# Optimization experiments

Measured on AMD Instinct MI355X. Metric: run time of the kernel, lower is better.

## Reference

```python
import jax, jax.numpy as jnp
import numpy as np

BETA = 0.25


def setup_inputs() -> dict:
    key = jax.random.key(0)
    k1, k2 = jax.random.split(key)
    z = jax.random.normal(k1, (16, 1024, 256), dtype=jnp.float32)
    embedding = jax.random.normal(k2, (8192, 256), dtype=jnp.float32)
    return {"z": z, "embedding": embedding}


def reference(z, embedding):
    e_dim = embedding.shape[-1]
    z_flat = jnp.reshape(z, (-1, e_dim))  # [N, e_dim]
    # d[i,k] = ||z_i||^2 + ||e_k||^2 - 2 z_i . e_k  -> [N, n_e]
    d = (jnp.sum(z_flat ** 2, axis=1, keepdims=True)
         + jnp.sum(embedding ** 2, axis=1)
         - 2.0 * jnp.einsum('nd,kd->nk', z_flat, embedding))
    min_encoding_indices = jnp.argmin(d, axis=1)  # [N]
    z_q = embedding[min_encoding_indices]
    z_q = jnp.reshape(z_q, z.shape)
    loss = (jnp.mean((jax.lax.stop_gradient(z_q) - z) ** 2)
            + BETA * jnp.mean((z_q - jax.lax.stop_gradient(z)) ** 2))
    z_q = z + jax.lax.stop_gradient(z_q - z)  # straight-through estimator
    return (z_q, loss, min_encoding_indices)
```

## Files before the change

kernel.cpp:

```cpp
#include <hip/hip_runtime.h>
#include <stdint.h>

#define N_ROWS   16384
#define DIM      256
#define N_CODES  8192
#define ZQ_ELEMS 4194304

typedef _Float16 f16x8 __attribute__((ext_vector_type(8)));
typedef _Float16 f16x4 __attribute__((ext_vector_type(4)));
typedef float    f32x16 __attribute__((ext_vector_type(16)));
typedef unsigned long long u64;

#define WS_ET  0
#define WS_PK  (8519680)

static __device__ __forceinline__ u64 packkey(float d, int c) {
    unsigned int u = __float_as_uint(d);
    u ^= ((unsigned int)((int)u >> 31)) | 0x80000000u;
    return ((u64)u << 32) | (unsigned int)c;
}

__global__ void vq_prep(const float* __restrict__ emb, _Float16* __restrict__ et,
                        u64* __restrict__ pkeys, float* __restrict__ loss_ptr) {
    __shared__ _Float16 sh[2][32][272];
    const int t = threadIdx.x, w = t >> 6, l = t & 63;
    if (blockIdx.x == 0 && t == 0) *loss_ptr = 0.0f;
    if (t < 64) pkeys[blockIdx.x * 64 + t] = ~0ULL;
    const int code0 = blockIdx.x * 32;
    const int sp0 = code0 >> 11, cw0 = code0 & 2047;
    #pragma unroll
    for (int j = 0; j < 8; ++j) {
        const int cl = w * 8 + j;
        float4 v = *(const float4*)(emb + (size_t)(code0 + cl) * DIM + l * 4);
        float xs[4] = {v.x, v.y, v.z, v.w};
        f16x4 hh, lo;
        float s = 0.0f;
        #pragma unroll
        for (int i = 0; i < 4; ++i) {
            _Float16 h = (_Float16)xs[i];
            hh[i] = h;
            lo[i] = (_Float16)(xs[i] - (float)h);
            s += xs[i] * xs[i];
        }
        *(f16x4*)&sh[0][cl][l * 4] = hh;
        *(f16x4*)&sh[1][cl][l * 4] = lo;
        #pragma unroll
        for (int off = 32; off > 0; off >>= 1) s += __shfl_down(s, off, 64);
        if (l == 0) {
            _Float16 nh = (_Float16)s;
            _Float16 nl = (_Float16)(s - (float)nh);
            f16x8 aug;
            #pragma unroll
            for (int i = 0; i < 8; ++i) aug[i] = (_Float16)0;
            aug[0] = nh; aug[1] = nl;
            *(f16x8*)(et + ((size_t)524288 + code0 + cl) * 8) = aug;
        }
    }
    __syncthreads();
    #pragma unroll
    for (int pp = 0; pp < 8; ++pp) {
        const int gi = pp * 256 + t;
        const int p = gi >> 10, ks = (gi >> 6) & 15, cl = (gi >> 1) & 31, h = gi & 1;
        f16x8 frag = *(const f16x8*)&sh[p][cl][ks * 16 + h * 8];
        const size_t unit = (size_t)p * 262144 + (size_t)sp0 * 65536
                          + (size_t)ks * 4096 + (size_t)(cw0 + cl) * 2 + h;
        *(f16x8*)(et + unit * 8) = frag;
    }
}

__global__ __launch_bounds__(512, 2)
void vq_main(const float* __restrict__ z, const _Float16* __restrict__ et,
             u64* __restrict__ pkeys) {
    extern __shared__ char smem[];
    u64* run = (u64*)(smem + 133120);

    const int tid = threadIdx.x;
    const int w = tid >> 6, L = tid & 63, lo5 = L & 31, hi1 = L >> 5;
    const int rb = blockIdx.x >> 2, sp = blockIdx.x & 3;
    const int row0 = rb * 128, codeS = sp * 2048;

    const float* zr = z + (size_t)row0 * DIM;
    #pragma unroll
    for (int jj = 0; jj < 16; ++jj) {
        const int idx = jj * 512 + tid;
        const int r = idx >> 6, q = idx & 63;
        float4 v = *(const float4*)(zr + (size_t)r * DIM + q * 4);
        float xs[4] = {v.x, v.y, v.z, v.w};
        f16x4 hh, lo;
        #pragma unroll
        for (int i = 0; i < 4; ++i) {
            const float m2 = -2.0f * xs[i];
            _Float16 h = (_Float16)m2;
            hh[i] = h;
            lo[i] = (_Float16)(m2 - (float)h);
        }
        char* base = smem + r * 1040 + q * 8;
        *(f16x4*)(base) = hh;
        *(f16x4*)(base + 512) = lo;
    }
    run[tid] = ~0ULL;
    run[tid + 512] = ~0ULL;

    f16x8 bz;
    #pragma unroll
    for (int i = 0; i < 8; ++i) bz[i] = (_Float16)0;
    if (hi1 == 0) { bz[0] = (_Float16)1; bz[1] = (_Float16)1; }

    f32x16 zacc;
    #pragma unroll
    for (int e = 0; e < 16; ++e) zacc[e] = 0.0f;

    const f16x8* eb  = (const f16x8*)et;
    const f16x8* ebL = eb + 262144;
    const int laneU = lo5 * 2 + hi1;
    const size_t spB = (size_t)sp * 65536;
    const char* zbA = smem + (lo5 * 1040 + hi1 * 16);
    const char* zbB = zbA + 66560;

    f16x8 paug[2];
    {
        const int c0 = codeS + w * 64;
        paug[0] = eb[(size_t)524288 + c0 + lo5];
        paug[1] = eb[(size_t)524288 + c0 + 32 + lo5];
    }
    f16x8 aC0, aC1, aC2, aC3;
    {
        const size_t cu = spB + (size_t)(w * 64) * 2 + laneU;
        aC0 = eb[cu]; aC1 = eb[cu + 64]; aC2 = ebL[cu]; aC3 = ebL[cu + 64];
    }
    __syncthreads();

    for (int ci = 0; ci < 4; ++ci) {
        const int c0 = codeS + ci * 512 + w * 64;
        const size_t cu = spB + (size_t)(ci * 512 + w * 64) * 2 + laneU;
        f32x16 acc[2][4];

        __builtin_amdgcn_s_setprio(1);
        #pragma unroll
        for (int mt = 0; mt < 2; ++mt)
            #pragma unroll
            for (int nt = 0; nt < 4; ++nt)
                acc[mt][nt] = __builtin_amdgcn_mfma_f32_32x32x16_f16(paug[mt], bz, zacc, 0, 0, 0);
        __builtin_amdgcn_s_setprio(0);

        if (ci < 3) {
            const int c1 = codeS + (ci + 1) * 512 + w * 64;
            paug[0] = eb[(size_t)524288 + c1 + lo5];
            paug[1] = eb[(size_t)524288 + c1 + 32 + lo5];
        }

        #pragma unroll 4
        for (int ksg = 0; ksg < 16; ++ksg) {
            const size_t ubn = cu + (size_t)(ksg + 1) * 4096;
            f16x8 aN0 = eb[ubn], aN1 = eb[ubn + 64];
            f16x8 aN2 = ebL[ubn], aN3 = ebL[ubn + 64];

            {
                f16x8 bh0 = *(const f16x8*)(zbA + (ksg * 32));
                f16x8 bl0 = *(const f16x8*)(zbA + (ksg * 32 + 512));
                f16x8 bh1 = *(const f16x8*)(zbA + (ksg * 32 + 33280));
                f16x8 bl1 = *(const f16x8*)(zbA + (ksg * 32 + 33280 + 512));
                __builtin_amdgcn_s_setprio(1);
                acc[0][0] = __builtin_amdgcn_mfma_f32_32x32x16_f16(aC0, bh0, acc[0][0], 0, 0, 0);
                acc[0][0] = __builtin_amdgcn_mfma_f32_32x32x16_f16(aC0, bl0, acc[0][0], 0, 0, 0);
                acc[0][0] = __builtin_amdgcn_mfma_f32_32x32x16_f16(aC2, bh0, acc[0][0], 0, 0, 0);
                acc[0][1] = __builtin_amdgcn_mfma_f32_32x32x16_f16(aC0, bh1, acc[0][1], 0, 0, 0);
                acc[0][1] = __builtin_amdgcn_mfma_f32_32x32x16_f16(aC0, bl1, acc[0][1], 0, 0, 0);
                acc[0][1] = __builtin_amdgcn_mfma_f32_32x32x16_f16(aC2, bh1, acc[0][1], 0, 0, 0);
                acc[1][0] = __builtin_amdgcn_mfma_f32_32x32x16_f16(aC1, bh0, acc[1][0], 0, 0, 0);
                acc[1][0] = __builtin_amdgcn_mfma_f32_32x32x16_f16(aC1, bl0, acc[1][0], 0, 0, 0);
                acc[1][0] = __builtin_amdgcn_mfma_f32_32x32x16_f16(aC3, bh0, acc[1][0], 0, 0, 0);
                acc[1][1] = __builtin_amdgcn_mfma_f32_32x32x16_f16(aC1, bh1, acc[1][1], 0, 0, 0);
                acc[1][1] = __builtin_amdgcn_mfma_f32_32x32x16_f16(aC1, bl1, acc[1][1], 0, 0, 0);
                acc[1][1] = __builtin_amdgcn_mfma_f32_32x32x16_f16(aC3, bh1, acc[1][1], 0, 0, 0);
                __builtin_amdgcn_s_setprio(0);
            }
            {
                f16x8 bh2 = *(const f16x8*)(zbB + (ksg * 32));
                f16x8 bl2 = *(const f16x8*)(zbB + (ksg * 32 + 512));
                f16x8 bh3 = *(const f16x8*)(zbB + (ksg * 32 + 33280));
                f16x8 bl3 = *(const f16x8*)(zbB + (ksg * 32 + 33280 + 512));
                __builtin_amdgcn_s_setprio(1);
                acc[0][2] = __builtin_amdgcn_mfma_f32_32x32x16_f16(aC0, bh2, acc[0][2], 0, 0, 0);
                acc[0][2] = __builtin_amdgcn_mfma_f32_32x32x16_f16(aC0, bl2, acc[0][2], 0, 0, 0);
                acc[0][2] = __builtin_amdgcn_mfma_f32_32x32x16_f16(aC2, bh2, acc[0][2], 0, 0, 0);
                acc[0][3] = __builtin_amdgcn_mfma_f32_32x32x16_f16(aC0, bh3, acc[0][3], 0, 0, 0);
                acc[0][3] = __builtin_amdgcn_mfma_f32_32x32x16_f16(aC0, bl3, acc[0][3], 0, 0, 0);
                acc[0][3] = __builtin_amdgcn_mfma_f32_32x32x16_f16(aC2, bh3, acc[0][3], 0, 0, 0);
                acc[1][2] = __builtin_amdgcn_mfma_f32_32x32x16_f16(aC1, bh2, acc[1][2], 0, 0, 0);
                acc[1][2] = __builtin_amdgcn_mfma_f32_32x32x16_f16(aC1, bl2, acc[1][2], 0, 0, 0);
                acc[1][2] = __builtin_amdgcn_mfma_f32_32x32x16_f16(aC3, bh2, acc[1][2], 0, 0, 0);
                acc[1][3] = __builtin_amdgcn_mfma_f32_32x32x16_f16(aC1, bh3, acc[1][3], 0, 0, 0);
                acc[1][3] = __builtin_amdgcn_mfma_f32_32x32x16_f16(aC1, bl3, acc[1][3], 0, 0, 0);
                acc[1][3] = __builtin_amdgcn_mfma_f32_32x32x16_f16(aC3, bh3, acc[1][3], 0, 0, 0);
                __builtin_amdgcn_s_setprio(0);
            }
            aC0 = aN0; aC1 = aN1; aC2 = aN2; aC3 = aN3;
        }

        {
            const size_t cuN = spB + (size_t)((((ci + 1) & 3) * 512) + w * 64) * 2 + laneU;
            aC0 = eb[cuN]; aC1 = eb[cuN + 64]; aC2 = ebL[cuN]; aC3 = ebL[cuN + 64];
        }

        #pragma unroll
        for (int nt = 0; nt < 4; ++nt) {
            float mm[16];
            #pragma unroll
            for (int r = 0; r < 16; ++r)
                mm[r] = fminf(acc[0][nt][r], acc[1][nt][r]);
            #pragma unroll
            for (int s2 = 8; s2 > 0; s2 >>= 1)
                #pragma unroll
                for (int r = 0; r < 8; ++r)
                    if (r < s2) mm[r] = fminf(mm[r], mm[r + s2]);
            const float m = mm[0];
            int rel = 64;
            #pragma unroll
            for (int mt = 0; mt < 2; ++mt)
                #pragma unroll
                for (int r = 0; r < 16; ++r) {
                    const int rc = mt * 32 + (r & 3) + 8 * (r >> 2);
                    const int cand = (acc[mt][nt][r] == m) ? rc : 64;
                    rel = cand < rel ? cand : rel;
                }
            u64 best = packkey(m, c0 + 4 * hi1 + rel);
            const u64 o = __shfl_xor(best, 32, 64);
            if (o < best) best = o;
            if (hi1 == 0) {
                u64* p = &run[w * 128 + nt * 32 + lo5];
                if (best < *p) *p = best;
            }
        }
    }

    __syncthreads();
    if (tid < 128) {
        u64 k = run[tid];
        #pragma unroll
        for (int w2 = 1; w2 < 8; ++w2) { u64 o = run[w2 * 128 + tid]; if (o < k) k = o; }
        atomicMin(&pkeys[row0 + tid], k);
    }
}

__global__ __launch_bounds__(512)
void vq_final(const float* __restrict__ z, const float* __restrict__ emb,
              const u64* __restrict__ pkeys,
              float* __restrict__ zq_out, float* __restrict__ loss_out,
              float* __restrict__ idx_out) {
    __shared__ int best[64];
    const int t = threadIdx.x;
    const int row0 = blockIdx.x * 64;
    if (t < 64) {
        const u64 k = pkeys[row0 + t];
        const int code = (int)(k & 0xFFFFFFFFu);
        best[t] = code;
        idx_out[row0 + t] = (float)code;
    }
    __syncthreads();
    const int wave = t >> 6, lane = t & 63;
    float lsum = 0.0f;
    #pragma unroll
    for (int rr = 0; rr < 8; ++rr) {
        const int rl = wave * 8 + rr;
        const int rg = row0 + rl;
        const int code = best[rl];
        float4 ev = *(const float4*)(emb + (size_t)code * DIM + lane * 4);
        float4 zv = *(const float4*)(z   + (size_t)rg   * DIM + lane * 4);
        float dx = ev.x - zv.x, dy = ev.y - zv.y;
        float dz = ev.z - zv.z, dw = ev.w - zv.w;
        lsum += dx * dx + dy * dy + dz * dz + dw * dw;
        *(float4*)(zq_out + (size_t)rg * DIM + lane * 4) = ev;
    }
    #pragma unroll
    for (int off = 32; off > 0; off >>= 1) lsum += __shfl_down(lsum, off, 64);
    if (lane == 0) atomicAdd(loss_out, lsum * (1.25f / (float)ZQ_ELEMS));
}

extern "C" void kernel_launch(void* const* d_in, const int* in_sizes, int n_in,
                              void* d_out, int out_size, void* d_ws, size_t ws_size,
                              hipStream_t stream) {
    const float* z   = (const float*)d_in[0];
    const float* emb = (const float*)d_in[1];
    float* out  = (float*)d_out;
    float* zq   = out;
    float* loss = out + ZQ_ELEMS;
    float* idx  = out + ZQ_ELEMS + 1;

    char* ws = (char*)d_ws;
    _Float16* et = (_Float16*)(ws + WS_ET);
    u64*   pk    = (u64*)(ws + WS_PK);

    static bool attr_set = false;
    if (!attr_set) {
        hipFuncSetAttribute((const void*)vq_main,
                            hipFuncAttributeMaxDynamicSharedMemorySize, 141312);
        attr_set = true;
    }

    vq_prep<<<256, 256, 0, stream>>>(emb, et, pk, loss);
    vq_main<<<512, 512, 141312, stream>>>(z, et, pk);
    vq_final<<<N_ROWS / 64, 512, 0, stream>>>(z, emb, pk, zq, loss, idx);
}
```

Baseline: 274.3 us.

## Fuse final gather/loss kernel into main kernel via last-block counter

Removes the separate vq_final launch: each row-block's four code-split blocks increment a per-row-block counter, and the last one to finish reads the merged argmin keys, writes indices, gathers the codebook rows into z_q and accumulates the loss. It rebuilds z from the split fp16 hi/lo copy already in shared memory instead of rereading it from global memory. This saves a kernel launch and the z reread, but adds a serialized tail in the last block and relies on memory fences so the other blocks' atomicMin results are visible.

```diff
diff --git a/kernel.cpp b/kernel.cpp
--- a/kernel.cpp
+++ b/kernel.cpp
@@ -13,6 +13,7 @@
 
 #define WS_ET  0
 #define WS_PK  (8519680)
+#define WS_CNT (8650752)
 
 static __device__ __forceinline__ u64 packkey(float d, int c) {
     unsigned int u = __float_as_uint(d);
@@ -21,10 +22,12 @@
 }
 
 __global__ void vq_prep(const float* __restrict__ emb, _Float16* __restrict__ et,
-                        u64* __restrict__ pkeys, float* __restrict__ loss_ptr) {
+                        u64* __restrict__ pkeys, unsigned int* __restrict__ cnt,
+                        float* __restrict__ loss_ptr) {
     __shared__ _Float16 sh[2][32][272];
     const int t = threadIdx.x, w = t >> 6, l = t & 63;
     if (blockIdx.x == 0 && t == 0) *loss_ptr = 0.0f;
+    if (t == 0 && blockIdx.x < 128) cnt[blockIdx.x] = 0;
     if (t < 64) pkeys[blockIdx.x * 64 + t] = ~0ULL;
     const int code0 = blockIdx.x * 32;
     const int sp0 = code0 >> 11, cw0 = code0 & 2047;
@@ -69,10 +72,14 @@
 }
 
 __global__ __launch_bounds__(512, 2)
-void vq_main(const float* __restrict__ z, const _Float16* __restrict__ et,
-             u64* __restrict__ pkeys) {
+void vq_main(const float* __restrict__ z, const float* __restrict__ emb,
+             const _Float16* __restrict__ et, u64* __restrict__ pkeys,
+             unsigned int* __restrict__ cnt,
+             float* __restrict__ zq_out, float* __restrict__ loss_out,
+             float* __restrict__ idx_out) {
     extern __shared__ char smem[];
     u64* run = (u64*)(smem + 133120);
+    int* bestc = (int*)(smem + 133120);
 
     const int tid = threadIdx.x;
     const int w = tid >> 6, L = tid & 63, lo5 = L & 31, hi1 = L >> 5;
@@ -241,40 +248,43 @@
         for (int w2 = 1; w2 < 8; ++w2) { u64 o = run[w2 * 128 + tid]; if (o < k) k = o; }
         atomicMin(&pkeys[row0 + tid], k);
     }
-}
-
-__global__ __launch_bounds__(512)
-void vq_final(const float* __restrict__ z, const float* __restrict__ emb,
-              const u64* __restrict__ pkeys,
-              float* __restrict__ zq_out, float* __restrict__ loss_out,
-              float* __restrict__ idx_out) {
-    __shared__ int best[64];
-    const int t = threadIdx.x;
-    const int row0 = blockIdx.x * 64;
-    if (t < 64) {
-        const u64 k = pkeys[row0 + t];
-        const int code = (int)(k & 0xFFFFFFFFu);
-        best[t] = code;
-        idx_out[row0 + t] = (float)code;
-    }
-    __syncthreads();
-    const int wave = t >> 6, lane = t & 63;
-    float lsum = 0.0f;
-    #pragma unroll
-    for (int rr = 0; rr < 8; ++rr) {
-        const int rl = wave * 8 + rr;
-        const int rg = row0 + rl;
-        const int code = best[rl];
-        float4 ev = *(const float4*)(emb + (size_t)code * DIM + lane * 4);
-        float4 zv = *(const float4*)(z   + (size_t)rg   * DIM + lane * 4);
-        float dx = ev.x - zv.x, dy = ev.y - zv.y;
-        float dz = ev.z - zv.z, dw = ev.w - zv.w;
-        lsum += dx * dx + dy * dy + dz * dz + dw * dw;
-        *(float4*)(zq_out + (size_t)rg * DIM + lane * 4) = ev;
-    }
-    #pragma unroll
-    for (int off = 32; off > 0; off >>= 1) lsum += __shfl_down(lsum, off, 64);
-    if (lane == 0) atomicAdd(loss_out, lsum * (1.25f / (float)ZQ_ELEMS));
+    asm volatile("s_waitcnt vmcnt(0)" ::: "memory");
+    __syncthreads();
+
+    __shared__ unsigned int lastold;
+    if (tid == 0) lastold = atomicAdd(&cnt[rb], 1u);
+    __syncthreads();
+    if (lastold == 3u) {
+        if (tid < 128) {
+            const u64 k = atomicMin(&pkeys[row0 + tid], ~0ULL);
+            const int code = (int)(k & 0xFFFFFFFFu);
+            bestc[tid] = code;
+            idx_out[row0 + tid] = (float)code;
+        }
+        __syncthreads();
+        float lsum = 0.0f;
+        #pragma unroll
+        for (int rr = 0; rr < 16; ++rr) {
+            const int rl = w * 16 + rr;
+            const int rg = row0 + rl;
+            const int code = bestc[rl];
+            float4 ev = *(const float4*)(emb + (size_t)code * DIM + L * 4);
+            const char* zrow = smem + rl * 1040 + (L >> 1) * 16 + (L & 1) * 8;
+            f16x4 hh = *(const f16x4*)(zrow);
+            f16x4 ll = *(const f16x4*)(zrow + 512);
+            float zx = -0.5f * ((float)hh[0] + (float)ll[0]);
+            float zy = -0.5f * ((float)hh[1] + (float)ll[1]);
+            float zz = -0.5f * ((float)hh[2] + (float)ll[2]);
+            float zw = -0.5f * ((float)hh[3] + (float)ll[3]);
+            float dx = ev.x - zx, dy = ev.y - zy;
+            float dz = ev.z - zz, dw = ev.w - zw;
+            lsum += dx * dx + dy * dy + dz * dz + dw * dw;
+            *(float4*)(zq_out + (size_t)rg * DIM + L * 4) = ev;
+        }
+        #pragma unroll
+        for (int off = 32; off > 0; off >>= 1) lsum += __shfl_down(lsum, off, 64);
+        if (L == 0) atomicAdd(loss_out, lsum * (1.25f / (float)ZQ_ELEMS));
+    }
 }
 
 extern "C" void kernel_launch(void* const* d_in, const int* in_sizes, int n_in,
@@ -290,6 +300,7 @@
     char* ws = (char*)d_ws;
     _Float16* et = (_Float16*)(ws + WS_ET);
     u64*   pk    = (u64*)(ws + WS_PK);
+    unsigned int* cn = (unsigned int*)(ws + WS_CNT);
 
     static bool attr_set = false;
     if (!attr_set) {
@@ -298,7 +309,6 @@
         attr_set = true;
     }
 
-    vq_prep<<<256, 256, 0, stream>>>(emb, et, pk, loss);
-    vq_main<<<512, 512, 141312, stream>>>(z, et, pk);
-    vq_final<<<N_ROWS / 64, 512, 0, stream>>>(z, emb, pk, zq, loss, idx);
+    vq_prep<<<256, 256, 0, stream>>>(emb, et, pk, cn, loss);
+    vq_main<<<512, 512, 141312, stream>>>(z, emb, et, pk, cn, zq, loss, idx);
 }
```

Measured after the change: 356.4 us. +29.9%, slower.

## Fuse prep, main and final into one cooperative persistent kernel

Applied to the files above, without the earlier changes.

Replaces the three kernel launches with a single cooperative kernel of 256 blocks that uses grid.sync between the embedding-prep, distance/argmin and gather/loss phases. Each block now processes two 128-row tiles in sequence, and the final phase reads keys through atomicMin, which also resets them. The intent is to remove launch gaps and tail effects between kernels. The cost is grid-wide barriers, half as many blocks resident during the main phase, and a dependence on all blocks being co-resident, since 256 blocks at 141 KB of LDS each must fit one per CU.

```diff
diff --git a/kernel.cpp b/kernel.cpp
--- a/kernel.cpp
+++ b/kernel.cpp
@@ -1,5 +1,8 @@
 #include <hip/hip_runtime.h>
+#include <hip/hip_cooperative_groups.h>
 #include <stdint.h>
+
+namespace cg = cooperative_groups;
 
 #define N_ROWS   16384
 #define DIM      256
@@ -20,86 +23,69 @@
     return ((u64)u << 32) | (unsigned int)c;
 }
 
-__global__ void vq_prep(const float* __restrict__ emb, _Float16* __restrict__ et,
-                        u64* __restrict__ pkeys, float* __restrict__ loss_ptr) {
-    __shared__ _Float16 sh[2][32][272];
-    const int t = threadIdx.x, w = t >> 6, l = t & 63;
-    if (blockIdx.x == 0 && t == 0) *loss_ptr = 0.0f;
-    if (t < 64) pkeys[blockIdx.x * 64 + t] = ~0ULL;
-    const int code0 = blockIdx.x * 32;
-    const int sp0 = code0 >> 11, cw0 = code0 & 2047;
-    #pragma unroll
-    for (int j = 0; j < 8; ++j) {
-        const int cl = w * 8 + j;
-        float4 v = *(const float4*)(emb + (size_t)(code0 + cl) * DIM + l * 4);
-        float xs[4] = {v.x, v.y, v.z, v.w};
-        f16x4 hh, lo;
-        float s = 0.0f;
-        #pragma unroll
-        for (int i = 0; i < 4; ++i) {
-            _Float16 h = (_Float16)xs[i];
-            hh[i] = h;
-            lo[i] = (_Float16)(xs[i] - (float)h);
-            s += xs[i] * xs[i];
-        }
-        *(f16x4*)&sh[0][cl][l * 4] = hh;
-        *(f16x4*)&sh[1][cl][l * 4] = lo;
-        #pragma unroll
-        for (int off = 32; off > 0; off >>= 1) s += __shfl_down(s, off, 64);
-        if (l == 0) {
-            _Float16 nh = (_Float16)s;
-            _Float16 nl = (_Float16)(s - (float)nh);
-            f16x8 aug;
-            #pragma unroll
-            for (int i = 0; i < 8; ++i) aug[i] = (_Float16)0;
-            aug[0] = nh; aug[1] = nl;
-            *(f16x8*)(et + ((size_t)524288 + code0 + cl) * 8) = aug;
-        }
+__global__ __launch_bounds__(512, 2)
+void vq_fused(const float* __restrict__ z, const float* __restrict__ emb,
+              _Float16* __restrict__ et, u64* __restrict__ pkeys,
+              float* __restrict__ zq_out, float* __restrict__ loss_out,
+              float* __restrict__ idx_out) {
+    extern __shared__ char smem[];
+    cg::grid_group grid = cg::this_grid();
+
+    const int t = threadIdx.x, w = t >> 6, L = t & 63;
+    const int lo5 = L & 31, hi1 = L >> 5;
+    const int rb = blockIdx.x >> 2, sp = blockIdx.x & 3;
+    const int codeS = sp * 2048;
+
+    {
+        _Float16* shp = (_Float16*)smem;
+        if (blockIdx.x == 0 && t == 0) *loss_out = 0.0f;
+        if (t < 64) pkeys[blockIdx.x * 64 + t] = ~0ULL;
+        const int code0 = blockIdx.x * 32;
+        const int sp0 = code0 >> 11, cw0 = code0 & 2047;
+        #pragma unroll
+        for (int j = 0; j < 4; ++j) {
+            const int cl = w * 4 + j;
+            float4 v = *(const float4*)(emb + (size_t)(code0 + cl) * DIM + L * 4);
+            float xs[4] = {v.x, v.y, v.z, v.w};
+            f16x4 hh, lo;
+            float s = 0.0f;
+            #pragma unroll
+            for (int i = 0; i < 4; ++i) {
+                _Float16 h = (_Float16)xs[i];
+                hh[i] = h;
+                lo[i] = (_Float16)(xs[i] - (float)h);
+                s += xs[i] * xs[i];
+            }
+            *(f16x4*)&shp[cl * 272 + L * 4] = hh;
+            *(f16x4*)&shp[8704 + cl * 272 + L * 4] = lo;
+            #pragma unroll
+            for (int off = 32; off > 0; off >>= 1) s += __shfl_down(s, off, 64);
+            if (L == 0) {
+                _Float16 nh = (_Float16)s;
+                _Float16 nl = (_Float16)(s - (float)nh);
+                f16x8 aug;
+                #pragma unroll
+                for (int i = 0; i < 8; ++i) aug[i] = (_Float16)0;
+                aug[0] = nh; aug[1] = nl;
+                *(f16x8*)(et + ((size_t)524288 + code0 + cl) * 8) = aug;
+            }
+        }
+        __syncthreads();
+        #pragma unroll
+        for (int pp = 0; pp < 4; ++pp) {
+            const int gi = pp * 512 + t;
+            const int p = gi >> 10, ks = (gi >> 6) & 15, cl = (gi >> 1) & 31, h = gi & 1;
+            f16x8 frag = *(const f16x8*)&shp[p * 8704 + cl * 272 + ks * 16 + h * 8];
+            const size_t unit = (size_t)p * 262144 + (size_t)sp0 * 65536
+                              + (size_t)ks * 4096 + (size_t)(cw0 + cl) * 2 + h;
+            *(f16x8*)(et + unit * 8) = frag;
+        }
+        __syncthreads();
+        if (w == 0) __threadfence();
     }
-    __syncthreads();
-    #pragma unroll
-    for (int pp = 0; pp < 8; ++pp) {
-        const int gi = pp * 256 + t;
-        const int p = gi >> 10, ks = (gi >> 6) & 15, cl = (gi >> 1) & 31, h = gi & 1;
-        f16x8 frag = *(const f16x8*)&sh[p][cl][ks * 16 + h * 8];
-        const size_t unit = (size_t)p * 262144 + (size_t)sp0 * 65536
-                          + (size_t)ks * 4096 + (size_t)(cw0 + cl) * 2 + h;
-        *(f16x8*)(et + unit * 8) = frag;
-    }
-}
-
-__global__ __launch_bounds__(512, 2)
-void vq_main(const float* __restrict__ z, const _Float16* __restrict__ et,
-             u64* __restrict__ pkeys) {
-    extern __shared__ char smem[];
+    grid.sync();
+
     u64* run = (u64*)(smem + 133120);
-
-    const int tid = threadIdx.x;
-    const int w = tid >> 6, L = tid & 63, lo5 = L & 31, hi1 = L >> 5;
-    const int rb = blockIdx.x >> 2, sp = blockIdx.x & 3;
-    const int row0 = rb * 128, codeS = sp * 2048;
-
-    const float* zr = z + (size_t)row0 * DIM;
-    #pragma unroll
-    for (int jj = 0; jj < 16; ++jj) {
-        const int idx = jj * 512 + tid;
-        const int r = idx >> 6, q = idx & 63;
-        float4 v = *(const float4*)(zr + (size_t)r * DIM + q * 4);
-        float xs[4] = {v.x, v.y, v.z, v.w};
-        f16x4 hh, lo;
-        #pragma unroll
-        for (int i = 0; i < 4; ++i) {
-            const float m2 = -2.0f * xs[i];
-            _Float16 h = (_Float16)m2;
-            hh[i] = h;
-            lo[i] = (_Float16)(m2 - (float)h);
-        }
-        char* base = smem + r * 1040 + q * 8;
-        *(f16x4*)(base) = hh;
-        *(f16x4*)(base + 512) = lo;
-    }
-    run[tid] = ~0ULL;
-    run[tid + 512] = ~0ULL;
 
     f16x8 bz;
     #pragma unroll
@@ -117,164 +103,194 @@
     const char* zbA = smem + (lo5 * 1040 + hi1 * 16);
     const char* zbB = zbA + 66560;
 
-    f16x8 paug[2];
+    for (int pi = 0; pi < 2; ++pi) {
+        const int row0 = (rb + 64 * pi) * 128;
+        __syncthreads();
+
+        const float* zr = z + (size_t)row0 * DIM;
+        #pragma unroll
+        for (int jj = 0; jj < 16; ++jj) {
+            const int idx = jj * 512 + t;
+            const int r = idx >> 6, q = idx & 63;
+            float4 v = *(const float4*)(zr + (size_t)r * DIM + q * 4);
+            float xs[4] = {v.x, v.y, v.z, v.w};
+            f16x4 hh, lo;
+            #pragma unroll
+            for (int i = 0; i < 4; ++i) {
+                const float m2 = -2.0f * xs[i];
+                _Float16 h = (_Float16)m2;
+                hh[i] = h;
+                lo[i] = (_Float16)(m2 - (float)h);
+            }
+            char* base = smem + r * 1040 + q * 8;
+            *(f16x4*)(base) = hh;
+            *(f16x4*)(base + 512) = lo;
+        }
+        run[t] = ~0ULL;
+        run[t + 512] = ~0ULL;
+
+        f16x8 paug[2];
+        {
+            const int c0 = codeS + w * 64;
+            paug[0] = eb[(size_t)524288 + c0 + lo5];
+            paug[1] = eb[(size_t)524288 + c0 + 32 + lo5];
+        }
+        f16x8 aC0, aC1, aC2, aC3;
+        {
+            const size_t cu = spB + (size_t)(w * 64) * 2 + laneU;
+            aC0 = eb[cu]; aC1 = eb[cu + 64]; aC2 = ebL[cu]; aC3 = ebL[cu + 64];
+        }
+        __syncthreads();
+
+        for (int ci = 0; ci < 4; ++ci) {
+            const int c0 = codeS + ci * 512 + w * 64;
+            const size_t cu = spB + (size_t)(ci * 512 + w * 64) * 2 + laneU;
+            f32x16 acc[2][4];
+
+            __builtin_amdgcn_s_setprio(1);
+            #pragma unroll
+            for (int mt = 0; mt < 2; ++mt)
+                #pragma unroll
+                for (int nt = 0; nt < 4; ++nt)
+                    acc[mt][nt] = __builtin_amdgcn_mfma_f32_32x32x16_f16(paug[mt], bz, zacc, 0, 0, 0);
+            __builtin_amdgcn_s_setprio(0);
+
+            if (ci < 3) {
+                const int c1 = codeS + (ci + 1) * 512 + w * 64;
+                paug[0] = eb[(size_t)524288 + c1 + lo5];
+                paug[1] = eb[(size_t)524288 + c1 + 32 + lo5];
+            }
+
+            #pragma unroll 4
+            for (int ksg = 0; ksg < 16; ++ksg) {
+                const size_t ubn = cu + (size_t)(ksg + 1) * 4096;
+                f16x8 aN0 = eb[ubn], aN1 = eb[ubn + 64];
+                f16x8 aN2 = ebL[ubn], aN3 = ebL[ubn + 64];
+
+                {
+                    f16x8 bh0 = *(const f16x8*)(zbA + (ksg * 32));
+                    f16x8 bl0 = *(const f16x8*)(zbA + (ksg * 32 + 512));
+                    f16x8 bh1 = *(const f16x8*)(zbA + (ksg * 32 + 33280));
+                    f16x8 bl1 = *(const f16x8*)(zbA + (ksg * 32 + 33280 + 512));
+                    __builtin_amdgcn_s_setprio(1);
+                    acc[0][0] = __builtin_amdgcn_mfma_f32_32x32x16_f16(aC0, bh0, acc[0][0], 0, 0, 0);
+                    acc[0][0] = __builtin_amdgcn_mfma_f32_32x32x16_f16(aC0, bl0, acc[0][0], 0, 0, 0);
+                    acc[0][0] = __builtin_amdgcn_mfma_f32_32x32x16_f16(aC2, bh0, acc[0][0], 0, 0, 0);
+                    acc[0][1] = __builtin_amdgcn_mfma_f32_32x32x16_f16(aC0, bh1, acc[0][1], 0, 0, 0);
+                    acc[0][1] = __builtin_amdgcn_mfma_f32_32x32x16_f16(aC0, bl1, acc[0][1], 0, 0, 0);
+                    acc[0][1] = __builtin_amdgcn_mfma_f32_32x32x16_f16(aC2, bh1, acc[0][1], 0, 0, 0);
+                    acc[1][0] = __builtin_amdgcn_mfma_f32_32x32x16_f16(aC1, bh0, acc[1][0], 0, 0, 0);
+                    acc[1][0] = __builtin_amdgcn_mfma_f32_32x32x16_f16(aC1, bl0, acc[1][0], 0, 0, 0);
+                    acc[1][0] = __builtin_amdgcn_mfma_f32_32x32x16_f16(aC3, bh0, acc[1][0], 0, 0, 0);
+                    acc[1][1] = __builtin_amdgcn_mfma_f32_32x32x16_f16(aC1, bh1, acc[1][1], 0, 0, 0);
+                    acc[1][1] = __builtin_amdgcn_mfma_f32_32x32x16_f16(aC1, bl1, acc[1][1], 0, 0, 0);
+                    acc[1][1] = __builtin_amdgcn_mfma_f32_32x32x16_f16(aC3, bh1, acc[1][1], 0, 0, 0);
+                    __builtin_amdgcn_s_setprio(0);
+                }
+                {
+                    f16x8 bh2 = *(const f16x8*)(zbB + (ksg * 32));
+                    f16x8 bl2 = *(const f16x8*)(zbB + (ksg * 32 + 512));
+                    f16x8 bh3 = *(const f16x8*)(zbB + (ksg * 32 + 33280));
+                    f16x8 bl3 = *(const f16x8*)(zbB + (ksg * 32 + 33280 + 512));
+                    __builtin_amdgcn_s_setprio(1);
+                    acc[0][2] = __builtin_amdgcn_mfma_f32_32x32x16_f16(aC0, bh2, acc[0][2], 0, 0, 0);
+                    acc[0][2] = __builtin_amdgcn_mfma_f32_32x32x16_f16(aC0, bl2, acc[0][2], 0, 0, 0);
+                    acc[0][2] = __builtin_amdgcn_mfma_f32_32x32x16_f16(aC2, bh2, acc[0][2], 0, 0, 0);
+                    acc[0][3] = __builtin_amdgcn_mfma_f32_32x32x16_f16(aC0, bh3, acc[0][3], 0, 0, 0);
+                    acc[0][3] = __builtin_amdgcn_mfma_f32_32x32x16_f16(aC0, bl3, acc[0][3], 0, 0, 0);
+                    acc[0][3] = __builtin_amdgcn_mfma_f32_32x32x16_f16(aC2, bh3, acc[0][3], 0, 0, 0);
+                    acc[1][2] = __builtin_amdgcn_mfma_f32_32x32x16_f16(aC1, bh2, acc[1][2], 0, 0, 0);
+                    acc[1][2] = __builtin_amdgcn_mfma_f32_32x32x16_f16(aC1, bl2, acc[1][2], 0, 0, 0);
+                    acc[1][2] = __builtin_amdgcn_mfma_f32_32x32x16_f16(aC3, bh2, acc[1][2], 0, 0, 0);
+                    acc[1][3] = __builtin_amdgcn_mfma_f32_32x32x16_f16(aC1, bh3, acc[1][3], 0, 0, 0);
+                    acc[1][3] = __builtin_amdgcn_mfma_f32_32x32x16_f16(aC1, bl3, acc[1][3], 0, 0, 0);
+                    acc[1][3] = __builtin_amdgcn_mfma_f32_32x32x16_f16(aC3, bh3, acc[1][3], 0, 0, 0);
+                    __builtin_amdgcn_s_setprio(0);
+                }
+                aC0 = aN0; aC1 = aN1; aC2 = aN2; aC3 = aN3;
+            }
+
+            {
+                const size_t cuN = spB + (size_t)((((ci + 1) & 3) * 512) + w * 64) * 2 + laneU;
+                aC0 = eb[cuN]; aC1 = eb[cuN + 64]; aC2 = ebL[cuN]; aC3 = ebL[cuN + 64];
+            }
+
+            #pragma unroll
+            for (int nt = 0; nt < 4; ++nt) {
+                float mm[16];
+                #pragma unroll
+                for (int r = 0; r < 16; ++r)
+                    mm[r] = fminf(acc[0][nt][r], acc[1][nt][r]);
+                #pragma unroll
+                for (int s2 = 8; s2 > 0; s2 >>= 1)
+                    #pragma unroll
+                    for (int r = 0; r < 8; ++r)
+                        if (r < s2) mm[r] = fminf(mm[r], mm[r + s2]);
+                const float m = mm[0];
+                int rel = 64;
+                #pragma unroll
+                for (int mt = 0; mt < 2; ++mt)
+                    #pragma unroll
+                    for (int r = 0; r < 16; ++r) {
+                        const int rc = mt * 32 + (r & 3) + 8 * (r >> 2);
+                        const int cand = (acc[mt][nt][r] == m) ? rc : 64;
+                        rel = cand < rel ? cand : rel;
+                    }
+                u64 best = packkey(m, c0 + 4 * hi1 + rel);
+                const u64 o = __shfl_xor(best, 32, 64);
+                if (o < best) best = o;
+                if (hi1 == 0) {
+                    u64* p = &run[w * 128 + nt * 32 + lo5];
+                    if (best < *p) *p = best;
+                }
+            }
+        }
+
+        __syncthreads();
+        if (t < 128) {
+            u64 k = run[t];
+            #pragma unroll
+            for (int w2 = 1; w2 < 8; ++w2) { u64 o = run[w2 * 128 + t]; if (o < k) k = o; }
+            atomicMin(&pkeys[row0 + t], k);
+        }
+    }
+    grid.sync();
+
     {
-        const int c0 = codeS + w * 64;
-        paug[0] = eb[(size_t)524288 + c0 + lo5];
-        paug[1] = eb[(size_t)524288 + c0 + 32 + lo5];
+        int* bestc = (int*)(smem + 133120);
+        float* wsum = (float*)(smem + 137216);
+        if (t < 64) {
+            const int gr = ((t < 32) ? rb * 128 : 8192 + rb * 128) + sp * 32 + (t & 31);
+            const u64 k = atomicMin(&pkeys[gr], ~0ULL);
+            const int code = (int)(k & 0xFFFFFFFFu);
+            bestc[t] = code;
+            idx_out[gr] = (float)code;
+        }
+        __syncthreads();
+        float lsum = 0.0f;
+        #pragma unroll
+        for (int rr = 0; rr < 8; ++rr) {
+            const int rl = w * 8 + rr;
+            const int gr = ((rl < 32) ? rb * 128 : 8192 + rb * 128) + sp * 32 + (rl & 31);
+            const int code = bestc[rl];
+            float4 ev = *(const float4*)(emb + (size_t)code * DIM + L * 4);
+            float4 zv = *(const float4*)(z   + (size_t)gr   * DIM + L * 4);
+            float dx = ev.x - zv.x, dy = ev.y - zv.y;
+            float dz = ev.z - zv.z, dw = ev.w - zv.w;
+            lsum += dx * dx + dy * dy + dz * dz + dw * dw;
+            *(float4*)(zq_out + (size_t)gr * DIM + L * 4) = ev;
+        }
+        #pragma unroll
+        for (int off = 32; off > 0; off >>= 1) lsum += __shfl_down(lsum, off, 64);
+        if (L == 0) wsum[w] = lsum;
+        __syncthreads();
+        if (t == 0) {
+            float s = 0.0f;
+            #pragma unroll
+            for (int i = 0; i < 8; ++i) s += wsum[i];
+            atomicAdd(loss_out, s * (1.25f / (float)ZQ_ELEMS));
+        }
     }
-    f16x8 aC0, aC1, aC2, aC3;
-    {
-        const size_t cu = spB + (size_t)(w * 64) * 2 + laneU;
-        aC0 = eb[cu]; aC1 = eb[cu + 64]; aC2 = ebL[cu]; aC3 = ebL[cu + 64];
-    }
-    __syncthreads();
-
-    for (int ci = 0; ci < 4; ++ci) {
-        const int c0 = codeS + ci * 512 + w * 64;
-        const size_t cu = spB + (size_t)(ci * 512 + w * 64) * 2 + laneU;
-        f32x16 acc[2][4];
-
-        __builtin_amdgcn_s_setprio(1);
-        #pragma unroll
-        for (int mt = 0; mt < 2; ++mt)
-            #pragma unroll
-            for (int nt = 0; nt < 4; ++nt)
-                acc[mt][nt] = __builtin_amdgcn_mfma_f32_32x32x16_f16(paug[mt], bz, zacc, 0, 0, 0);
-        __builtin_amdgcn_s_setprio(0);
-
-        if (ci < 3) {
-            const int c1 = codeS + (ci + 1) * 512 + w * 64;
-            paug[0] = eb[(size_t)524288 + c1 + lo5];
-            paug[1] = eb[(size_t)524288 + c1 + 32 + lo5];
-        }
-
-        #pragma unroll 4
-        for (int ksg = 0; ksg < 16; ++ksg) {
-            const size_t ubn = cu + (size_t)(ksg + 1) * 4096;
-            f16x8 aN0 = eb[ubn], aN1 = eb[ubn + 64];
-            f16x8 aN2 = ebL[ubn], aN3 = ebL[ubn + 64];
-
-            {
-                f16x8 bh0 = *(const f16x8*)(zbA + (ksg * 32));
-                f16x8 bl0 = *(const f16x8*)(zbA + (ksg * 32 + 512));
-                f16x8 bh1 = *(const f16x8*)(zbA + (ksg * 32 + 33280));
-                f16x8 bl1 = *(const f16x8*)(zbA + (ksg * 32 + 33280 + 512));
-                __builtin_amdgcn_s_setprio(1);
-                acc[0][0] = __builtin_amdgcn_mfma_f32_32x32x16_f16(aC0, bh0, acc[0][0], 0, 0, 0);
-                acc[0][0] = __builtin_amdgcn_mfma_f32_32x32x16_f16(aC0, bl0, acc[0][0], 0, 0, 0);
-                acc[0][0] = __builtin_amdgcn_mfma_f32_32x32x16_f16(aC2, bh0, acc[0][0], 0, 0, 0);
-                acc[0][1] = __builtin_amdgcn_mfma_f32_32x32x16_f16(aC0, bh1, acc[0][1], 0, 0, 0);
-                acc[0][1] = __builtin_amdgcn_mfma_f32_32x32x16_f16(aC0, bl1, acc[0][1], 0, 0, 0);
-                acc[0][1] = __builtin_amdgcn_mfma_f32_32x32x16_f16(aC2, bh1, acc[0][1], 0, 0, 0);
-                acc[1][0] = __builtin_amdgcn_mfma_f32_32x32x16_f16(aC1, bh0, acc[1][0], 0, 0, 0);
-                acc[1][0] = __builtin_amdgcn_mfma_f32_32x32x16_f16(aC1, bl0, acc[1][0], 0, 0, 0);
-                acc[1][0] = __builtin_amdgcn_mfma_f32_32x32x16_f16(aC3, bh0, acc[1][0], 0, 0, 0);
-                acc[1][1] = __builtin_amdgcn_mfma_f32_32x32x16_f16(aC1, bh1, acc[1][1], 0, 0, 0);
-                acc[1][1] = __builtin_amdgcn_mfma_f32_32x32x16_f16(aC1, bl1, acc[1][1], 0, 0, 0);
-                acc[1][1] = __builtin_amdgcn_mfma_f32_32x32x16_f16(aC3, bh1, acc[1][1], 0, 0, 0);
-                __builtin_amdgcn_s_setprio(0);
-            }
-            {
-                f16x8 bh2 = *(const f16x8*)(zbB + (ksg * 32));
-                f16x8 bl2 = *(const f16x8*)(zbB + (ksg * 32 + 512));
-                f16x8 bh3 = *(const f16x8*)(zbB + (ksg * 32 + 33280));
-                f16x8 bl3 = *(const f16x8*)(zbB + (ksg * 32 + 33280 + 512));
-                __builtin_amdgcn_s_setprio(1);
-                acc[0][2] = __builtin_amdgcn_mfma_f32_32x32x16_f16(aC0, bh2, acc[0][2], 0, 0, 0);
-                acc[0][2] = __builtin_amdgcn_mfma_f32_32x32x16_f16(aC0, bl2, acc[0][2], 0, 0, 0);
-                acc[0][2] = __builtin_amdgcn_mfma_f32_32x32x16_f16(aC2, bh2, acc[0][2], 0, 0, 0);
-                acc[0][3] = __builtin_amdgcn_mfma_f32_32x32x16_f16(aC0, bh3, acc[0][3], 0, 0, 0);
-                acc[0][3] = __builtin_amdgcn_mfma_f32_32x32x16_f16(aC0, bl3, acc[0][3], 0, 0, 0);
-                acc[0][3] = __builtin_amdgcn_mfma_f32_32x32x16_f16(aC2, bh3, acc[0][3], 0, 0, 0);
-                acc[1][2] = __builtin_amdgcn_mfma_f32_32x32x16_f16(aC1, bh2, acc[1][2], 0, 0, 0);
-                acc[1][2] = __builtin_amdgcn_mfma_f32_32x32x16_f16(aC1, bl2, acc[1][2], 0, 0, 0);
-                acc[1][2] = __builtin_amdgcn_mfma_f32_32x32x16_f16(aC3, bh2, acc[1][2], 0, 0, 0);
-                acc[1][3] = __builtin_amdgcn_mfma_f32_32x32x16_f16(aC1, bh3, acc[1][3], 0, 0, 0);
-                acc[1][3] = __builtin_amdgcn_mfma_f32_32x32x16_f16(aC1, bl3, acc[1][3], 0, 0, 0);
-                acc[1][3] = __builtin_amdgcn_mfma_f32_32x32x16_f16(aC3, bh3, acc[1][3], 0, 0, 0);
-                __builtin_amdgcn_s_setprio(0);
-            }
-            aC0 = aN0; aC1 = aN1; aC2 = aN2; aC3 = aN3;
-        }
-
-        {
-            const size_t cuN = spB + (size_t)((((ci + 1) & 3) * 512) + w * 64) * 2 + laneU;
-            aC0 = eb[cuN]; aC1 = eb[cuN + 64]; aC2 = ebL[cuN]; aC3 = ebL[cuN + 64];
-        }
-
-        #pragma unroll
-        for (int nt = 0; nt < 4; ++nt) {
-            float mm[16];
-            #pragma unroll
-            for (int r = 0; r < 16; ++r)
-                mm[r] = fminf(acc[0][nt][r], acc[1][nt][r]);
-            #pragma unroll
-            for (int s2 = 8; s2 > 0; s2 >>= 1)
-                #pragma unroll
-                for (int r = 0; r < 8; ++r)
-                    if (r < s2) mm[r] = fminf(mm[r], mm[r + s2]);
-            const float m = mm[0];
-            int rel = 64;
-            #pragma unroll
-            for (int mt = 0; mt < 2; ++mt)
-                #pragma unroll
-                for (int r = 0; r < 16; ++r) {
-                    const int rc = mt * 32 + (r & 3) + 8 * (r >> 2);
-                    const int cand = (acc[mt][nt][r] == m) ? rc : 64;
-                    rel = cand < rel ? cand : rel;
-                }
-            u64 best = packkey(m, c0 + 4 * hi1 + rel);
-            const u64 o = __shfl_xor(best, 32, 64);
-            if (o < best) best = o;
-            if (hi1 == 0) {
-                u64* p = &run[w * 128 + nt * 32 + lo5];
-                if (best < *p) *p = best;
-            }
-        }
-    }
-
-    __syncthreads();
-    if (tid < 128) {
-        u64 k = run[tid];
-        #pragma unroll
-        for (int w2 = 1; w2 < 8; ++w2) { u64 o = run[w2 * 128 + tid]; if (o < k) k = o; }
-        atomicMin(&pkeys[row0 + tid], k);
-    }
-}
-
-__global__ __launch_bounds__(512)
-void vq_final(const float* __restrict__ z, const float* __restrict__ emb,
-              const u64* __restrict__ pkeys,
-              float* __restrict__ zq_out, float* __restrict__ loss_out,
-              float* __restrict__ idx_out) {
-    __shared__ int best[64];
-    const int t = threadIdx.x;
-    const int row0 = blockIdx.x * 64;
-    if (t < 64) {
-        const u64 k = pkeys[row0 + t];
-        const int code = (int)(k & 0xFFFFFFFFu);
-        best[t] = code;
-        idx_out[row0 + t] = (float)code;
-    }
-    __syncthreads();
-    const int wave = t >> 6, lane = t & 63;
-    float lsum = 0.0f;
-    #pragma unroll
-    for (int rr = 0; rr < 8; ++rr) {
-        const int rl = wave * 8 + rr;
-        const int rg = row0 + rl;
-        const int code = best[rl];
-        float4 ev = *(const float4*)(emb + (size_t)code * DIM + lane * 4);
-        float4 zv = *(const float4*)(z   + (size_t)rg   * DIM + lane * 4);
-        float dx = ev.x - zv.x, dy = ev.y - zv.y;
-        float dz = ev.z - zv.z, dw = ev.w - zv.w;
-        lsum += dx * dx + dy * dy + dz * dz + dw * dw;
-        *(float4*)(zq_out + (size_t)rg * DIM + lane * 4) = ev;
-    }
-    #pragma unroll
-    for (int off = 32; off > 0; off >>= 1) lsum += __shfl_down(lsum, off, 64);
-    if (lane == 0) atomicAdd(loss_out, lsum * (1.25f / (float)ZQ_ELEMS));
 }
 
 extern "C" void kernel_launch(void* const* d_in, const int* in_sizes, int n_in,
@@ -293,12 +309,13 @@
 
     static bool attr_set = false;
     if (!attr_set) {
-        hipFuncSetAttribute((const void*)vq_main,
+        hipFuncSetAttribute((const void*)vq_fused,
                             hipFuncAttributeMaxDynamicSharedMemorySize, 141312);
         attr_set = true;
     }
 
-    vq_prep<<<256, 256, 0, stream>>>(emb, et, pk, loss);
-    vq_main<<<512, 512, 141312, stream>>>(z, et, pk);
-    vq_final<<<N_ROWS / 64, 512, 0, stream>>>(z, emb, pk, zq, loss, idx);
+    void* args[] = {(void*)&z, (void*)&emb, (void*)&et, (void*)&pk,
+                    (void*)&zq, (void*)&loss, (void*)&idx};
+    hipLaunchCooperativeKernel((const void*)vq_fused, dim3(256), dim3(512),
+                               args, 141312, stream);
 }
```

Result: slower. 333.1 us (+21.4%).
